# Kernel optimization log

Measured on AMD Instinct MI355X. Metric: run time of the kernel, lower is better.

The kernel has to match this reference:

```python
import jax, jax.numpy as jnp
import numpy as np

B, N, D = 2, 2048, 1024
H, QH, DH = 8, 16, 64        # kv heads, query heads, head dim
SOFTCLAMP = 50.0


def setup_inputs() -> dict:
    key = jax.random.key(0)
    ks = jax.random.split(key, 7)
    return {
        "tokens": jax.random.normal(ks[0], (B, N, D), jnp.float32),
        "norm_w": jnp.ones((D,), jnp.float32) + 0.02 * jax.random.normal(ks[1], (D,), jnp.float32),
        "Wq":  0.02 * jax.random.normal(ks[2], (D, QH * DH), jnp.float32),
        "Wkv": 0.02 * jax.random.normal(ks[3], (D, 2 * H * DH), jnp.float32),
        "Wout": 0.02 * jax.random.normal(ks[4], (H * DH, D), jnp.float32),
        "q_gamma": 0.02 * jax.random.normal(ks[5], (QH, DH), jnp.float32),
        "k_gamma": 0.02 * jax.random.normal(ks[6], (H, DH), jnp.float32),
    }


def _rmsnorm(x, w):
    eps = jnp.finfo(x.dtype).eps
    return x * jax.lax.rsqrt(jnp.mean(x * x, axis=-1, keepdims=True) + eps) * w


def _l2norm(x):
    # F.normalize(dim=-1, p=2) clamps the norm at eps=1e-12
    n = jnp.maximum(jnp.linalg.norm(x, axis=-1, keepdims=True), 1e-12)
    return x / n


def _mh_rmsnorm(x, gamma):
    # x: [b, h, n, d]; gamma: [h, d]; scale = (gamma + 1) * sqrt(d)
    scale = (gamma + 1.0) * np.sqrt(x.shape[-1]).astype(np.float32)
    return _l2norm(x) * scale[None, :, None, :]


def reference(tokens, norm_w, Wq, Wkv, Wout, q_gamma, k_gamma):
    b, n, d = tokens.shape
    x = _rmsnorm(tokens, norm_w)

    q = (x @ Wq).reshape(b, n, QH, DH).transpose(0, 2, 1, 3)      # [b, QH, n, dh]
    kv = x @ Wkv
    k = kv[..., : H * DH].reshape(b, n, H, DH).transpose(0, 2, 1, 3)  # [b, H, n, dh]
    v = kv[..., H * DH:].reshape(b, n, H, DH).transpose(0, 2, 1, 3)   # [b, H, n, dh]

    q = _mh_rmsnorm(q, q_gamma)
    k = _mh_rmsnorm(k, k_gamma)

    g = QH // H
    q = q.reshape(b, H, g, n, DH)                                 # [b, h, g, i, dh]

    sim = jnp.einsum('bhgid,bhjd->bhgij', q, k)                   # [b, h, g, i, j]
    sim = jnp.tanh(sim / SOFTCLAMP) * SOFTCLAMP                   # softcap BEFORE scale (faithful)
    sim = sim * (DH ** -0.5)

    neg = -jnp.finfo(sim.dtype).max
    causal = jnp.triu(jnp.ones((n, n), dtype=bool), 1)
    sim = jnp.where(causal, neg, sim)

    attn = jax.nn.softmax(sim, axis=-1)
    # NOTE: original einsum sums over the group axis g -> [b, h, i, dh]
    out = jnp.einsum('bhgij,bhjd->bhid', attn, v)
    out = out.transpose(0, 2, 1, 3).reshape(b, n, H * DH)
    return out @ Wout
```

## Files before the change

### kernel.cpp

```cpp
#include <hip/hip_runtime.h>
#include <hip/hip_bf16.h>
#include <type_traits>

typedef unsigned short u16;
typedef __attribute__((ext_vector_type(2))) float f32x2;
typedef __attribute__((ext_vector_type(4))) float f32x4;
typedef __attribute__((ext_vector_type(8))) short short8;
typedef __attribute__((ext_vector_type(4))) short short4v;
typedef __attribute__((ext_vector_type(8))) __bf16 bf16x8;
typedef __attribute__((ext_vector_type(4))) __bf16 bf16x4;

#define BB 2
#define NN 2048
#define DDIM 1024
#define HH 8
#define QHH 16
#define DHH 64

__device__ __forceinline__ float b2f(u16 v) {
    return __builtin_bit_cast(float, ((unsigned)v) << 16);
}
__device__ __forceinline__ u16 f2b(float f) {
    unsigned u = __builtin_bit_cast(unsigned, f);
    u += 0x7FFFu + ((u >> 16) & 1u);
    return (u16)(u >> 16);
}
__device__ __forceinline__ float fastrcp(float x) {
#if __has_builtin(__builtin_amdgcn_rcpf)
    return __builtin_amdgcn_rcpf(x);
#else
    return 1.0f / x;
#endif
}
__device__ __forceinline__ float fastexp2(float x) {
#if __has_builtin(__builtin_amdgcn_exp2f)
    return __builtin_amdgcn_exp2f(x);
#else
    return exp2f(x);
#endif
}
__device__ __forceinline__ f32x2 sp2(float v) { return (f32x2){v, v}; }
__device__ __forceinline__ f32x4 mfma16(short8 a, short8 b, f32x4 c) {
    return __builtin_amdgcn_mfma_f32_16x16x32_bf16(
        __builtin_bit_cast(bf16x8, a), __builtin_bit_cast(bf16x8, b), c, 0, 0, 0);
}
#if __has_builtin(__builtin_amdgcn_mfma_f32_16x16x16_bf16)
__device__ __forceinline__ f32x4 mfma_k16(short4v a, short4v b, f32x4 c) {
    return __builtin_amdgcn_mfma_f32_16x16x16_bf16(
        __builtin_bit_cast(bf16x4, a), __builtin_bit_cast(bf16x4, b), c, 0, 0, 0);
}
#else
__device__ __forceinline__ f32x4 mfma_k16(short4v a, short4v b, f32x4 c) {
    return __builtin_amdgcn_mfma_f32_16x16x16bf16_1k(a, b, c, 0, 0, 0);
}
#endif
__device__ __forceinline__ void stage16(const u16* g, u16* l, int lane) {
#if __has_builtin(__builtin_amdgcn_global_load_lds)
    __builtin_amdgcn_global_load_lds(
        (const __attribute__((address_space(1))) unsigned int*)g,
        (__attribute__((address_space(3))) unsigned int*)l, 16, 0, 0);
#else
    *(short8*)(l + lane * 8) = *(const short8*)g;
#endif
}

__global__ __launch_bounds__(256) void k_rmsnorm(const float* __restrict__ tokens,
                                                 const float* __restrict__ norm_w,
                                                 u16* __restrict__ xb) {
    const int row = blockIdx.x;
    const int tid = threadIdx.x;
    const float* xp = tokens + (size_t)row * DDIM + tid * 4;
    float4 raw = *(const float4*)xp;
    float ss = raw.x * raw.x + raw.y * raw.y + raw.z * raw.z + raw.w * raw.w;
#pragma unroll
    for (int d = 1; d < 64; d <<= 1) ss += __shfl_xor(ss, d);
    __shared__ float red[4];
    if ((tid & 63) == 0) red[tid >> 6] = ss;
    __syncthreads();
    float tot = red[0] + red[1] + red[2] + red[3];
    float r = rsqrtf(tot * (1.0f / 1024.0f) + 1.1920929e-7f);
    float4 wv = *(const float4*)(norm_w + tid * 4);
    ushort4 o;
    o.x = f2b(raw.x * r * wv.x);
    o.y = f2b(raw.y * r * wv.y);
    o.z = f2b(raw.z * r * wv.z);
    o.w = f2b(raw.w * r * wv.w);
    *(ushort4*)(xb + (size_t)row * DDIM + tid * 4) = o;
}

__global__ __launch_bounds__(256) void k_wprep(const float* __restrict__ Wq,
                                               const float* __restrict__ Wkv,
                                               const float* __restrict__ Wout,
                                               u16* __restrict__ WqT,
                                               u16* __restrict__ WkvT,
                                               u16* __restrict__ WoutT) {
    const int z = blockIdx.z;
    const float* in = (z == 0) ? Wq : (z == 1) ? Wkv : Wout;
    u16* out = (z == 0) ? WqT : (z == 1) ? WkvT : WoutT;
    const int R = (z == 2) ? 512 : 1024, C = 1024;
    const int br = blockIdx.y * 32;
    if (br >= R) return;
    __shared__ u16 tile[32][33];
    const int bc = blockIdx.x * 32;
    const int tx = threadIdx.x & 31, ty = threadIdx.x >> 5;
#pragma unroll
    for (int i = 0; i < 32; i += 8) tile[ty + i][tx] = f2b(in[(size_t)(br + ty + i) * C + bc + tx]);
    __syncthreads();
#pragma unroll
    for (int i = 0; i < 32; i += 8) out[(size_t)(bc + ty + i) * R + br + tx] = tile[tx][ty + i];
}

__global__ __launch_bounds__(256) void k_gemm128(const u16* __restrict__ A,
                                                 const u16* __restrict__ Bt,
                                                 u16* __restrict__ C,
                                                 int M, int Ncols, int K) {
    __shared__ __attribute__((aligned(16))) u16 As[128 * 32];
    __shared__ __attribute__((aligned(16))) u16 Bs[128 * 32];
    const int tid = threadIdx.x;
    const int lane = tid & 63;
    const int w = tid >> 6;
    const int m0 = blockIdx.y * 128;
    const int n0 = blockIdx.x * 128;
    const int wr = (w >> 1) * 64;
    const int wc = (w & 1) * 64;
    const int lr = lane & 15;
    const int lq = lane >> 4;

    const int ch0 = w * 32;
    const u16* aSrc = A + (size_t)(m0 + ch0 + (lane >> 2)) * K + (lane & 3) * 8;
    const u16* bSrc = Bt + (size_t)(n0 + ch0 + (lane >> 2)) * K + (lane & 3) * 8;
    u16* aDst = As + ch0 * 32;
    u16* bDst = Bs + ch0 * 32;

    f32x4 acc[4][4];
#pragma unroll
    for (int i = 0; i < 4; i++)
#pragma unroll
        for (int j = 0; j < 4; j++) acc[i][j] = (f32x4){0.f, 0.f, 0.f, 0.f};

    for (int k0 = 0; k0 < K; k0 += 32) {
        __syncthreads();
        stage16(aSrc, aDst, lane);
        stage16(aSrc + (size_t)16 * K, aDst + 512, lane);
        stage16(bSrc, bDst, lane);
        stage16(bSrc + (size_t)16 * K, bDst + 512, lane);
        aSrc += 32;
        bSrc += 32;
        __syncthreads();
        short8 a[4], b[4];
#pragma unroll
        for (int mi = 0; mi < 4; ++mi) a[mi] = *(const short8*)&As[(wr + mi * 16 + lr) * 32 + lq * 8];
#pragma unroll
        for (int ni = 0; ni < 4; ++ni) b[ni] = *(const short8*)&Bs[(wc + ni * 16 + lr) * 32 + lq * 8];
#pragma unroll
        for (int mi = 0; mi < 4; ++mi)
#pragma unroll
            for (int ni = 0; ni < 4; ++ni) acc[mi][ni] = mfma16(a[mi], b[ni], acc[mi][ni]);
    }
#pragma unroll
    for (int mi = 0; mi < 4; ++mi)
#pragma unroll
        for (int ni = 0; ni < 4; ++ni)
#pragma unroll
            for (int r = 0; r < 4; ++r) {
                int row = m0 + wr + mi * 16 + lq * 4 + r;
                int col = n0 + wc + ni * 16 + lr;
                C[(size_t)row * Ncols + col] = f2b(acc[mi][ni][r]);
            }
}

__global__ __launch_bounds__(256) void k_gemm64f(const u16* __restrict__ A,
                                                 const u16* __restrict__ Bt,
                                                 float* __restrict__ C,
                                                 int M, int Ncols, int K) {
    __shared__ __attribute__((aligned(16))) u16 As[64 * 32];
    __shared__ __attribute__((aligned(16))) u16 Bs[128 * 32];
    const int tid = threadIdx.x;
    const int lane = tid & 63;
    const int w = tid >> 6;
    const int m0 = blockIdx.y * 64;
    const int n0 = blockIdx.x * 128;
    const int lr = lane & 15;
    const int lq = lane >> 4;

    const u16* aSrc = A + (size_t)(m0 + w * 16 + (lane >> 2)) * K + (lane & 3) * 8;
    const u16* bSrc = Bt + (size_t)(n0 + w * 32 + (lane >> 2)) * K + (lane & 3) * 8;
    u16* aDst = As + w * 16 * 32;
    u16* bDst = Bs + w * 32 * 32;

    f32x4 acc[8];
#pragma unroll
    for (int i = 0; i < 8; i++) acc[i] = (f32x4){0.f, 0.f, 0.f, 0.f};

    for (int k0 = 0; k0 < K; k0 += 32) {
        __syncthreads();
        stage16(aSrc, aDst, lane);
        stage16(bSrc, bDst, lane);
        stage16(bSrc + (size_t)16 * K, bDst + 512, lane);
        aSrc += 32;
        bSrc += 32;
        __syncthreads();
        short8 a = *(const short8*)&As[(w * 16 + lr) * 32 + lq * 8];
#pragma unroll
        for (int nt = 0; nt < 8; ++nt) {
            short8 b = *(const short8*)&Bs[(nt * 16 + lr) * 32 + lq * 8];
            acc[nt] = mfma16(a, b, acc[nt]);
        }
    }
#pragma unroll
    for (int nt = 0; nt < 8; ++nt)
#pragma unroll
        for (int r = 0; r < 4; ++r) {
            int row = m0 + w * 16 + lq * 4 + r;
            int col = n0 + nt * 16 + lr;
            C[(size_t)row * Ncols + col] = acc[nt][r];
        }
}

__global__ __launch_bounds__(256) void k_headnorm(const u16* __restrict__ qkv,
                                                  const float* __restrict__ q_gamma,
                                                  const float* __restrict__ k_gamma,
                                                  u16* __restrict__ qn,
                                                  u16* __restrict__ kn) {
    const int row = blockIdx.x;
    const int b = row >> 11, n = row & 2047;
    const int lane = threadIdx.x & 63, w = threadIdx.x >> 6;
    const u16* qr = qkv + (size_t)row * 2048;
    const u16* kvr = qkv + (size_t)row * 2048 + 1024;
#pragma unroll
    for (int t = 0; t < 4; ++t) {
        int qh = w * 4 + t;
        float v = b2f(qr[qh * 64 + lane]);
        float ss = v * v;
#pragma unroll
        for (int d = 1; d < 64; d <<= 1) ss += __shfl_xor(ss, d);
        float nrm = fmaxf(sqrtf(ss), 1e-12f);
        float g = q_gamma[qh * 64 + lane];
        qn[((size_t)(b * QHH + qh) * NN + n) * 64 + lane] = f2b(v / nrm * (g + 1.0f) * 8.0f);
    }
#pragma unroll
    for (int t = 0; t < 2; ++t) {
        int kh = w * 2 + t;
        float v = b2f(kvr[kh * 64 + lane]);
        float ss = v * v;
#pragma unroll
        for (int d = 1; d < 64; d <<= 1) ss += __shfl_xor(ss, d);
        float nrm = fmaxf(sqrtf(ss), 1e-12f);
        float g = k_gamma[kh * 64 + lane];
        kn[((size_t)(b * HH + kh) * NN + n) * 64 + lane] = f2b(v / nrm * (g + 1.0f) * 0.16f);
    }
}

__global__ __launch_bounds__(256) void k_vtrans(const u16* __restrict__ qkv,
                                                u16* __restrict__ vt) {
    const int bh = blockIdx.x;
    const int b = bh >> 3, h = bh & 7;
    const int n0 = blockIdx.y * 64;
    const int tid = threadIdx.x;
    __shared__ u16 t[64 * 72];
#pragma unroll
    for (int it = 0; it < 2; ++it) {
        int idx = tid + it * 256;
        int i = idx >> 3, c = idx & 7;
        short8 v = *(const short8*)&qkv[(size_t)(b * NN + n0 + i) * 2048 + 1536 + h * 64 + c * 8];
        *(short8*)&t[i * 72 + c * 8] = v;
    }
    __syncthreads();
#pragma unroll
    for (int it = 0; it < 2; ++it) {
        int idx = tid + it * 256;
        int d = idx >> 3, c = idx & 7;
        u16 tmp[8];
#pragma unroll
        for (int j = 0; j < 8; ++j) tmp[j] = t[(c * 8 + j) * 72 + d];
        *(short8*)&vt[((size_t)(bh * 64 + d)) * NN + n0 + c * 8] = *(short8*)tmp;
    }
}

__global__ __launch_bounds__(256) void k_attn(const u16* __restrict__ qn,
                                              const u16* __restrict__ kn,
                                              const u16* __restrict__ vt,
                                              u16* __restrict__ OT) {
    const int bq = blockIdx.x;
    const int b = bq >> 4, qh = bq & 15;
    const int h = qh >> 1;
    const int tid = threadIdx.x;
    const int lane = tid & 63, w = tid >> 6;
    const int lr = lane & 15, lq = lane >> 4;
    const int z = 31 - blockIdx.y;
    const int i0 = z * 64 + w * 16;
    const int ntile = z + 1;
    const int irow = i0 + lr;

    const u16* Qp = qn + (size_t)(b * QHH + qh) * NN * 64;
    const u16* Kp = kn + (size_t)(b * HH + h) * NN * 64;
    const u16* Vp = vt + (size_t)(b * HH + h) * 64 * NN;
    u16* Op = OT + (size_t)(b * QHH + qh) * 64 * NN;

    __shared__ __attribute__((aligned(16))) u16 Ks[2][64 * 64];
    __shared__ __attribute__((aligned(16))) u16 Vs[2][64 * 64];

    short8 qf0 = *(const short8*)&Qp[(size_t)(i0 + lr) * 64 + lq * 8];
    short8 qf1 = *(const short8*)&Qp[(size_t)(i0 + lr) * 64 + 32 + lq * 8];

    f32x4 of[4];
#pragma unroll
    for (int dt = 0; dt < 4; ++dt) of[dt] = (f32x4){0.f, 0.f, 0.f, 0.f};
    f32x2 ls = {0.f, 0.f};

    const int srow = lane >> 3;
    const int sch = (lane ^ srow) & 7;
    const int rA = w * 16, rB = w * 16 + 8;

    const u16* kSrcA = Kp + (size_t)(rA + srow) * 64 + sch * 8;
    const u16* kSrcB = Kp + (size_t)(rB + srow) * 64 + sch * 8;
    const u16* vSrcA = Vp + (size_t)(rA + srow) * NN + sch * 8;
    const u16* vSrcB = Vp + (size_t)(rB + srow) * NN + sch * 8;

    auto stageKV = [&](int buf) {
        stage16(kSrcA, &Ks[buf][rA * 64], lane);
        stage16(kSrcB, &Ks[buf][rB * 64], lane);
        stage16(vSrcA, &Vs[buf][rA * 64], lane);
        stage16(vSrcB, &Vs[buf][rB * 64], lane);
        kSrcA += 64 * 64;
        kSrcB += 64 * 64;
        vSrcA += 64;
        vSrcB += 64;
    };

    auto smax = [&](f32x4 sc, int lim, bool masked) -> short4v {
        f32x2 xa = {sc[0], sc[1]};
        f32x2 xb = {sc[2], sc[3]};
        f32x2 ya = xa * xa;
        f32x2 yb = xb * xb;
        f32x2 Ga = __builtin_elementwise_fma(ya, __builtin_elementwise_fma(ya,
                       __builtin_elementwise_fma(ya, __builtin_elementwise_fma(ya,
                           sp2(0.04705711f), sp2(-0.32327190f)), sp2(1.11500760f)),
                       sp2(-2.98719110f)), sp2(9.01599730f));
        f32x2 Gb = __builtin_elementwise_fma(yb, __builtin_elementwise_fma(yb,
                       __builtin_elementwise_fma(yb, __builtin_elementwise_fma(yb,
                           sp2(0.04705711f), sp2(-0.32327190f)), sp2(1.11500760f)),
                       sp2(-2.98719110f)), sp2(9.01599730f));
        f32x2 aa = __builtin_elementwise_fma(xa, Ga, sp2(-9.0168440f));
        f32x2 ab = __builtin_elementwise_fma(xb, Gb, sp2(-9.0168440f));
        float p0 = fastexp2(aa.x);
        float p1 = fastexp2(aa.y);
        float p2 = fastexp2(ab.x);
        float p3 = fastexp2(ab.y);
        if (masked) {
            p0 = (0 <= lim) ? p0 : 0.0f;
            p1 = (1 <= lim) ? p1 : 0.0f;
            p2 = (2 <= lim) ? p2 : 0.0f;
            p3 = (3 <= lim) ? p3 : 0.0f;
        }
        ls += (f32x2){p0, p1};
        ls += (f32x2){p2, p3};
        bf16x4 pb;
        pb[0] = (__bf16)p0;
        pb[1] = (__bf16)p1;
        pb[2] = (__bf16)p2;
        pb[3] = (__bf16)p3;
        return __builtin_bit_cast(short4v, pb);
    };

    auto tile = [&](int buf, int jt) {
        const int j0 = jt << 6;
        const u16* kb = &Ks[buf][0];
        const u16* vb = &Vs[buf][0];
        f32x4 sc[4];
#pragma unroll
        for (int ct = 0; ct < 4; ++ct) {
            const int r = ct * 16 + lr;
            short8 kf0 = *(const short8*)&kb[r * 64 + ((lq ^ (lr & 7)) << 3)];
            short8 kf1 = *(const short8*)&kb[r * 64 + (((4 + lq) ^ (lr & 7)) << 3)];
            f32x4 t = (f32x4){0.f, 0.f, 0.f, 0.f};
            t = mfma16(kf0, qf0, t);
            t = mfma16(kf1, qf1, t);
            sc[ct] = t;
        }
        const bool masked = (jt == ntile - 1);
        short4v pk[4];
#pragma unroll
        for (int ct = 0; ct < 4; ++ct) {
            const int lim = irow - (j0 + ct * 16 + lq * 4);
            pk[ct] = smax(sc[ct], lim, masked);
        }
#pragma unroll
        for (int dt = 0; dt < 4; ++dt) {
            const int d = dt * 16 + lr;
#pragma unroll
            for (int ct = 0; ct < 4; ++ct) {
                short4v vf = *(const short4v*)
                    &vb[d * 64 + ((((ct << 1) + (lq >> 1)) ^ (lr & 7)) << 3) + ((lq & 1) << 2)];
                of[dt] = mfma_k16(vf, pk[ct], of[dt]);
            }
        }
    };

    stageKV(0);
    for (int jt = 0; jt < ntile; ++jt) {
        const int buf = jt & 1;
        __syncthreads();
        if (jt + 1 < ntile) stageKV(buf ^ 1);
        tile(buf, jt);
    }

    float l = ls.x + ls.y;
    l += __shfl_xor(l, 16);
    l += __shfl_xor(l, 32);
    const float inv = fastrcp(l);
#pragma unroll
    for (int dt = 0; dt < 4; ++dt)
#pragma unroll
        for (int r = 0; r < 4; ++r)
            Op[(size_t)(dt * 16 + lq * 4 + r) * NN + irow] = f2b(of[dt][r] * inv);
}

__global__ __launch_bounds__(256) void k_gsum(const u16* __restrict__ OT, u16* __restrict__ AO) {
    __shared__ u16 t[32][34];
    const int b = blockIdx.z;
    const int n0 = blockIdx.x * 32;
    const int c0 = blockIdx.y * 32;
    const int hh = c0 >> 6, d0 = c0 & 63;
    const int tx = threadIdx.x & 31, ty = threadIdx.x >> 5;
    const u16* O0 = OT + ((size_t)(b * QHH + 2 * hh) * 64 + d0) * NN;
    const u16* O1 = OT + ((size_t)(b * QHH + 2 * hh + 1) * 64 + d0) * NN;
#pragma unroll
    for (int i = ty; i < 32; i += 8)
        t[i][tx] = f2b(b2f(O0[(size_t)i * NN + n0 + tx]) + b2f(O1[(size_t)i * NN + n0 + tx]));
    __syncthreads();
#pragma unroll
    for (int i = ty; i < 32; i += 8)
        AO[((size_t)(b * NN) + n0 + i) * 512 + c0 + tx] = t[tx][i];
}

extern "C" void kernel_launch(void* const* d_in, const int* in_sizes, int n_in,
                              void* d_out, int out_size, void* d_ws, size_t ws_size,
                              hipStream_t stream) {
    const float* tokens = (const float*)d_in[0];
    const float* norm_w = (const float*)d_in[1];
    const float* Wq = (const float*)d_in[2];
    const float* Wkv = (const float*)d_in[3];
    const float* Wout = (const float*)d_in[4];
    const float* q_gamma = (const float*)d_in[5];
    const float* k_gamma = (const float*)d_in[6];
    float* out = (float*)d_out;

    char* ws = (char*)d_ws;
    u16* xb = (u16*)(ws + 0);
    u16* WqT = (u16*)(ws + 8388608);
    u16* WkvT = (u16*)(ws + 10485760);
    u16* WoutT = (u16*)(ws + 12582912);
    u16* qkv = (u16*)(ws + 13631488);
    u16* kn = (u16*)(ws + 30408704);
    u16* vtb = (u16*)(ws + 34603008);
    u16* qn = xb;
    u16* Obuf = qkv;
    u16* AO = (u16*)(ws + 22020096);

    k_rmsnorm<<<4096, 256, 0, stream>>>(tokens, norm_w, xb);
    k_wprep<<<dim3(32, 32, 3), 256, 0, stream>>>(Wq, Wkv, Wout, WqT, WkvT, WoutT);
    k_gemm128<<<dim3(16, 32), 256, 0, stream>>>(xb, WqT, qkv, 4096, 2048, 1024);
    k_headnorm<<<4096, 256, 0, stream>>>(qkv, q_gamma, k_gamma, qn, kn);
    k_vtrans<<<dim3(16, 32), 256, 0, stream>>>(qkv, vtb);
    k_attn<<<dim3(32, 32), 256, 0, stream>>>(qn, kn, vtb, Obuf);
    k_gsum<<<dim3(64, 16, 2), 256, 0, stream>>>(Obuf, AO);
    k_gemm64f<<<dim3(8, 64), 256, 0, stream>>>(AO, WoutT, out, 4096, 1024, 512);
}
```

Before: 188.3 us.

## Store attention output row-major, simplify group-sum, swizzle V, add MFMA priority

The attention kernel now writes its output row-major ([n][64]) with vector stores instead of scattered transposed scalar stores. That lets the group-sum kernel become a simple vectorized elementwise add with no shared-memory transpose. The V transpose kernel swizzles half-chunks and the attention V read applies the matching XOR, which is meant to cut LDS bank conflicts. s_setprio is raised around the MFMA sections to favour matrix issue across waves.

```diff
diff --git a/kernel.cpp b/kernel.cpp
--- a/kernel.cpp
+++ b/kernel.cpp
@@ -270,10 +270,13 @@
     for (int it = 0; it < 2; ++it) {
         int idx = tid + it * 256;
         int d = idx >> 3, c = idx & 7;
-        u16 tmp[8];
+        const int sw = (d >> 3) & 1;
+        u16 tmp[8], o[8];
 #pragma unroll
         for (int j = 0; j < 8; ++j) tmp[j] = t[(c * 8 + j) * 72 + d];
-        *(short8*)&vt[((size_t)(bh * 64 + d)) * NN + n0 + c * 8] = *(short8*)tmp;
+#pragma unroll
+        for (int j = 0; j < 8; ++j) o[j] = tmp[j ^ (sw << 2)];
+        *(short8*)&vt[((size_t)(bh * 64 + d)) * NN + n0 + c * 8] = *(short8*)o;
     }
 }
 
@@ -295,7 +298,7 @@
     const u16* Qp = qn + (size_t)(b * QHH + qh) * NN * 64;
     const u16* Kp = kn + (size_t)(b * HH + h) * NN * 64;
     const u16* Vp = vt + (size_t)(b * HH + h) * 64 * NN;
-    u16* Op = OT + (size_t)(b * QHH + qh) * 64 * NN;
+    u16* Op = OT + (size_t)(b * QHH + qh) * NN * 64;
 
     __shared__ __attribute__((aligned(16))) u16 Ks[2][64 * 64];
     __shared__ __attribute__((aligned(16))) u16 Vs[2][64 * 64];
@@ -368,6 +371,7 @@
         const u16* kb = &Ks[buf][0];
         const u16* vb = &Vs[buf][0];
         f32x4 sc[4];
+        __builtin_amdgcn_s_setprio(1);
 #pragma unroll
         for (int ct = 0; ct < 4; ++ct) {
             const int r = ct * 16 + lr;
@@ -378,6 +382,7 @@
             t = mfma16(kf1, qf1, t);
             sc[ct] = t;
         }
+        __builtin_amdgcn_s_setprio(0);
         const bool masked = (jt == ntile - 1);
         short4v pk[4];
 #pragma unroll
@@ -385,16 +390,19 @@
             const int lim = irow - (j0 + ct * 16 + lq * 4);
             pk[ct] = smax(sc[ct], lim, masked);
         }
+        __builtin_amdgcn_s_setprio(1);
 #pragma unroll
         for (int dt = 0; dt < 4; ++dt) {
             const int d = dt * 16 + lr;
 #pragma unroll
             for (int ct = 0; ct < 4; ++ct) {
                 short4v vf = *(const short4v*)
-                    &vb[d * 64 + ((((ct << 1) + (lq >> 1)) ^ (lr & 7)) << 3) + ((lq & 1) << 2)];
+                    &vb[d * 64 + ((((ct << 1) + (lq >> 1)) ^ (lr & 7)) << 3) +
+                        (((lq ^ (lr >> 3)) & 1) << 2)];
                 of[dt] = mfma_k16(vf, pk[ct], of[dt]);
             }
         }
+        __builtin_amdgcn_s_setprio(0);
     };
 
     stageKV(0);
@@ -410,28 +418,29 @@
     l += __shfl_xor(l, 32);
     const float inv = fastrcp(l);
 #pragma unroll
-    for (int dt = 0; dt < 4; ++dt)
-#pragma unroll
-        for (int r = 0; r < 4; ++r)
-            Op[(size_t)(dt * 16 + lq * 4 + r) * NN + irow] = f2b(of[dt][r] * inv);
-}
-
-__global__ __launch_bounds__(256) void k_gsum(const u16* __restrict__ OT, u16* __restrict__ AO) {
-    __shared__ u16 t[32][34];
-    const int b = blockIdx.z;
-    const int n0 = blockIdx.x * 32;
-    const int c0 = blockIdx.y * 32;
-    const int hh = c0 >> 6, d0 = c0 & 63;
-    const int tx = threadIdx.x & 31, ty = threadIdx.x >> 5;
-    const u16* O0 = OT + ((size_t)(b * QHH + 2 * hh) * 64 + d0) * NN;
-    const u16* O1 = OT + ((size_t)(b * QHH + 2 * hh + 1) * 64 + d0) * NN;
-#pragma unroll
-    for (int i = ty; i < 32; i += 8)
-        t[i][tx] = f2b(b2f(O0[(size_t)i * NN + n0 + tx]) + b2f(O1[(size_t)i * NN + n0 + tx]));
-    __syncthreads();
-#pragma unroll
-    for (int i = ty; i < 32; i += 8)
-        AO[((size_t)(b * NN) + n0 + i) * 512 + c0 + tx] = t[tx][i];
+    for (int dt = 0; dt < 4; ++dt) {
+        u16 o[4];
+#pragma unroll
+        for (int r = 0; r < 4; ++r) o[r] = f2b(of[dt][r] * inv);
+        *(ushort4*)&Op[(size_t)irow * 64 + dt * 16 + lq * 4] = *(ushort4*)o;
+    }
+}
+
+__global__ __launch_bounds__(256) void k_gsum(const u16* __restrict__ O, u16* __restrict__ AO) {
+    const int idx = blockIdx.x * 256 + threadIdx.x;
+    const int c8 = idx & 63;
+    const int n = (idx >> 6) & 2047;
+    const int b = idx >> 17;
+    const int hh = c8 >> 3;
+    const u16* p0 = O + (((size_t)(b * QHH + 2 * hh) * NN) + n) * 64 + (c8 & 7) * 8;
+    const u16* p1 = O + (((size_t)(b * QHH + 2 * hh + 1) * NN) + n) * 64 + (c8 & 7) * 8;
+    short8 a = *(const short8*)p0;
+    short8 c = *(const short8*)p1;
+    u16 o[8];
+#pragma unroll
+    for (int j = 0; j < 8; ++j)
+        o[j] = f2b(b2f((u16)a[j]) + b2f((u16)c[j]));
+    *(short8*)&AO[((size_t)(b * NN + n)) * 512 + c8 * 8] = *(short8*)o;
 }
 
 extern "C" void kernel_launch(void* const* d_in, const int* in_sizes, int n_in,
@@ -464,6 +473,6 @@
     k_headnorm<<<4096, 256, 0, stream>>>(qkv, q_gamma, k_gamma, qn, kn);
     k_vtrans<<<dim3(16, 32), 256, 0, stream>>>(qkv, vtb);
     k_attn<<<dim3(32, 32), 256, 0, stream>>>(qn, kn, vtb, Obuf);
-    k_gsum<<<dim3(64, 16, 2), 256, 0, stream>>>(Obuf, AO);
+    k_gsum<<<1024, 256, 0, stream>>>(Obuf, AO);
     k_gemm64f<<<dim3(8, 64), 256, 0, stream>>>(AO, WoutT, out, 4096, 1024, 512);
 }
```

After: 186.0 us. Within noise of the previous version (-1.2%).
